# Performance work log

Hardware: AMD Instinct MI355X
Metric: run time of the kernel (lower is better)

## Reference

```python
import jax, jax.numpy as jnp
import numpy as np

N_NODES = 50000
N_EDGES = 800000
IN_DIM = 50
HIDDEN = 256
N_CLASSES = 121
EPS = 1e-12


def setup_inputs() -> dict:
    key = jax.random.key(0)
    ks = jax.random.split(key, 12)
    p = lambda i, shape: (jax.random.normal(ks[i], shape, dtype=jnp.float32) * 0.05)
    x = jax.random.normal(ks[0], (N_NODES, IN_DIM), dtype=jnp.float32)
    edge_index = jax.random.randint(ks[1], (2, N_EDGES), 0, N_NODES, dtype=jnp.int64)
    return {
        "x": x,
        "edge_index": edge_index,
        # SAGEConv layer 1: lin_l (aggregated, with bias), lin_r (root, no bias)
        "w1_l": p(2, (IN_DIM, HIDDEN)), "b1": p(3, (HIDDEN,)), "w1_r": p(4, (IN_DIM, HIDDEN)),
        # parallel Linear 1
        "wl1": p(5, (IN_DIM, HIDDEN)), "bl1": p(6, (HIDDEN,)),
        # SAGEConv layer 2
        "w2_l": p(7, (HIDDEN, N_CLASSES)), "b2": p(8, (N_CLASSES,)), "w2_r": p(9, (HIDDEN, N_CLASSES)),
        # parallel Linear 2
        "wl2": p(10, (HIDDEN, N_CLASSES)), "bl2": p(11, (N_CLASSES,)),
    }


def _sage_conv(x, src, dst, w_l, b, w_r):
    # mean-aggregate source features at destination nodes (PyG SAGEConv, aggr='mean')
    n = x.shape[0]
    agg = jax.ops.segment_sum(x[src], dst, num_segments=n)            # [N, d]
    deg = jax.ops.segment_sum(jnp.ones((src.shape[0], 1), x.dtype), dst, num_segments=n)
    mean = agg / jnp.maximum(deg, 1.0)
    out = mean @ w_l + b + x @ w_r
    # normalize=True -> L2 row normalization (F.normalize semantics)
    norm = jnp.sqrt(jnp.sum(out * out, axis=-1, keepdims=True))
    return out / jnp.maximum(norm, EPS)


def reference(x, edge_index, w1_l, b1, w1_r, wl1, bl1, w2_l, b2, w2_r, wl2, bl2):
    src, dst = edge_index[0], edge_index[1]
    h = jax.nn.elu(_sage_conv(x, src, dst, w1_l, b1, w1_r) + (x @ wl1 + bl1))
    out = _sage_conv(h, src, dst, w2_l, b2, w2_r) + (h @ wl2 + bl2)
    return out
```

## Files before the change

### kernel.cpp

```cpp
#include <hip/hip_runtime.h>
#include <hip/hip_bf16.h>
#include <math.h>

typedef __hip_bfloat16 bf16;
typedef __attribute__((ext_vector_type(8))) short short8;
typedef __attribute__((ext_vector_type(4))) float f32x4;

#define N_NODES 50000
#define N_EDGES 800000
#define IN_DIM 50
#define HIDDEN 256
#define NCLS 121
#define PSTR 128
#define LDSPITCH 264
#define NCHUNK 196
#define P2ROWS 64
#define P1ROWS 32
#define P1PITCH 261
#define FEDGE 1024

#define OFF_OFF   50048
#define OFF_CSR   150160
#define OFF_HB    950272
#define OFF_PB    7350272
#define OFF_AB    10550272
#define OFF_QRB   15000272
#define OFF_QLB   18200272
#define OFF_BW    21400272
#define OFF_BW1   21449424
#define OFF_CSUM  21482240

__device__ __forceinline__ int clampi(int v, int hi) {
    return v < 0 ? 0 : (v >= hi ? hi - 1 : v);
}

__device__ __forceinline__ float uf(unsigned u) { return __uint_as_float(u); }

__global__ __launch_bounds__(256) void prep_r21(
    const float* __restrict__ x, bf16* __restrict__ xbp, bf16* __restrict__ ab,
    const float* __restrict__ w1l, const float* __restrict__ w1r,
    const float* __restrict__ wl1, bf16* __restrict__ bw1,
    const float* __restrict__ w2l, const float* __restrict__ w2r,
    const float* __restrict__ wl2, bf16* __restrict__ bw,
    int* __restrict__ degi) {
    int b = blockIdx.x;
    if (b < 25000) {
        int i = b * 256 + threadIdx.x;
        int n = i >> 7, c = i & 127;
        float v = 0.0f;
        if (c >= 64 && c < 64 + IN_DIM) v = x[n * IN_DIM + (c - 64)];
        ab[i] = __float2bfloat16(v);
        if (c < 64) {
            float xv = (c < IN_DIM) ? x[n * IN_DIM + c] : 0.0f;
            xbp[n * 64 + c] = __float2bfloat16(xv);
        }
    } else if (b < 25256) {
        int i = (b - 25000) * 256 + threadIdx.x;
        int kt = i / 16384, r = i % 16384, c = r / 32, t32 = r % 32;
        int q = t32 >> 3, j = t32 & 7;
        int k = kt * 32 + q * 8 + j;
        float v = 0.0f;
        if (k < 64) {
            if (k < IN_DIM && c < 256) v = w1l[k * HIDDEN + c];
        } else {
            int kr = k - 64;
            if (kr < IN_DIM)
                v = (c < 256) ? w1r[kr * HIDDEN + c] : wl1[kr * HIDDEN + (c - 256)];
        }
        bw1[i] = __float2bfloat16(v);
    } else if (b < 25640) {
        int i = (b - 25256) * 256 + threadIdx.x;
        int kt = i / 12288, r = i % 12288, c = r / 32, t32 = r % 32;
        int q = t32 >> 3, j = t32 & 7;
        int k = kt * 32 + q * 8 + j;
        int mat = c >> 7, cls = c & 127;
        float v = 0.0f;
        if (cls < NCLS) {
            const float* w = (mat == 0) ? w2l : ((mat == 1) ? w2r : wl2);
            v = w[k * NCLS + cls];
        }
        bw[i] = __float2bfloat16(v);
    } else {
        int i = (b - 25640) * 256 + threadIdx.x;
        if (i < N_NODES) degi[i] = 0;
    }
}

__global__ __launch_bounds__(256) void degrank_r21(const int* __restrict__ dst,
                                                   int* __restrict__ degi,
                                                   int* __restrict__ rank) {
    int e = blockIdx.x * 256 + threadIdx.x;
    if (e < N_EDGES) {
        int d = clampi(dst[e], N_NODES);
        rank[e] = atomicAdd(&degi[d], 1);
    }
}

__global__ __launch_bounds__(256) void chunksum_r21(const int* __restrict__ degi,
                                                    int* __restrict__ csum) {
    __shared__ int red[256];
    int i = blockIdx.x * 256 + threadIdx.x;
    red[threadIdx.x] = (i < N_NODES) ? degi[i] : 0;
    __syncthreads();
    for (int s = 128; s > 0; s >>= 1) {
        if (threadIdx.x < s) red[threadIdx.x] += red[threadIdx.x + s];
        __syncthreads();
    }
    if (threadIdx.x == 0) csum[blockIdx.x] = red[0];
}

__global__ __launch_bounds__(256) void scanscatter_r21(const int* __restrict__ csum,
                                                       const int* __restrict__ degi,
                                                       int* __restrict__ off) {
    __shared__ int cs[256];
    __shared__ int s[256];
    int t = threadIdx.x;
    int cv = (t < NCHUNK) ? csum[t] : 0;
    cs[t] = cv;
    __syncthreads();
    for (int d = 1; d < 256; d <<= 1) {
        int u = (t >= d) ? cs[t - d] : 0;
        __syncthreads();
        cs[t] += u;
        __syncthreads();
    }
    int cb = cs[blockIdx.x] - csum[blockIdx.x];
    if (blockIdx.x == 0 && t == 0) off[N_NODES] = cs[NCHUNK - 1];
    int i = blockIdx.x * 256 + t;
    int dv = (i < N_NODES) ? degi[i] : 0;
    s[t] = dv;
    __syncthreads();
    for (int d = 1; d < 256; d <<= 1) {
        int u = (t >= d) ? s[t - d] : 0;
        __syncthreads();
        s[t] += u;
        __syncthreads();
    }
    if (i < N_NODES) off[i] = s[t] - dv + cb;
}

__global__ __launch_bounds__(256) void csrfill2_r21(const int* __restrict__ src,
                                                    const int* __restrict__ dst,
                                                    const int* __restrict__ rank,
                                                    const int* __restrict__ off,
                                                    int* __restrict__ csr) {
    int e = blockIdx.x * 256 + threadIdx.x;
    if (e >= N_EDGES) return;
    int d = clampi(dst[e], N_NODES);
    csr[off[d] + rank[e]] = clampi(src[e], N_NODES);
}

__global__ __launch_bounds__(256) void gather1_r21(
    const uint2* __restrict__ xb2, const int* __restrict__ off,
    const int* __restrict__ csr, const int* __restrict__ degi,
    unsigned int* __restrict__ abu) {
    __shared__ float rdeg[8];
    __shared__ int soff[9];
    __shared__ int sidx[FEDGE];
    int base = blockIdx.x * 8;
    int tid = threadIdx.x;
    if (tid < 9) soff[tid] = off[base + tid];
    if (tid < 8) rdeg[tid] = 1.0f / fmaxf((float)degi[base + tid], 1.0f);
    __syncthreads();
    int e0b = soff[0];
    int count = soff[8] - e0b;
    bool inl = (count <= FEDGE);
    if (inl)
        for (int i = tid; i < count; i += 256) sidx[i] = csr[e0b + i];
    __syncthreads();

    int wave = tid >> 6, lane = tid & 63;
    int half = lane >> 5;
    int grp = (lane >> 4) & 1;
    int lg = lane & 15;
    int n = wave * 2 + half;
    int node = base + n;
    int e0 = soff[n], e1 = soff[n + 1];
    float a0 = 0, a1 = 0, a2 = 0, a3 = 0;
    float b0 = 0, b1 = 0, b2 = 0, b3 = 0;
    int e = e0;
    for (; e + 4 <= e1; e += 4) {
        int r0 = inl ? sidx[e + grp - e0b] : csr[e + grp];
        int r1 = inl ? sidx[e + 2 + grp - e0b] : csr[e + 2 + grp];
        uint2 u0 = xb2[(size_t)r0 * 16 + lg];
        uint2 u1 = xb2[(size_t)r1 * 16 + lg];
        a0 += uf(u0.x << 16);
        a1 += uf(u0.x & 0xffff0000u);
        a2 += uf(u0.y << 16);
        a3 += uf(u0.y & 0xffff0000u);
        b0 += uf(u1.x << 16);
        b1 += uf(u1.x & 0xffff0000u);
        b2 += uf(u1.y << 16);
        b3 += uf(u1.y & 0xffff0000u);
    }
    for (; e < e1; e += 2) {
        int idx = e + grp;
        int safe = idx < e1 ? idx : e;
        int r0 = inl ? sidx[safe - e0b] : csr[safe];
        uint2 u0 = xb2[(size_t)r0 * 16 + lg];
        if (idx < e1) {
            a0 += uf(u0.x << 16);
            a1 += uf(u0.x & 0xffff0000u);
            a2 += uf(u0.y << 16);
            a3 += uf(u0.y & 0xffff0000u);
        }
    }
    a0 += b0;
    a1 += b1;
    a2 += b2;
    a3 += b3;
    a0 += __shfl_xor(a0, 16, 64);
    a1 += __shfl_xor(a1, 16, 64);
    a2 += __shfl_xor(a2, 16, 64);
    a3 += __shfl_xor(a3, 16, 64);
    if (grp == 0) {
        float r = rdeg[n];
        bf16 v0 = __float2bfloat16(a0 * r), v1 = __float2bfloat16(a1 * r);
        bf16 v2 = __float2bfloat16(a2 * r), v3 = __float2bfloat16(a3 * r);
        unsigned p0 = (unsigned)*(unsigned short*)&v0 |
                      ((unsigned)*(unsigned short*)&v1 << 16);
        unsigned p1 = (unsigned)*(unsigned short*)&v2 |
                      ((unsigned)*(unsigned short*)&v3 << 16);
        abu[(size_t)node * 64 + 2 * lg] = p0;
        abu[(size_t)node * 64 + 2 * lg + 1] = p1;
    }
}

__global__ __launch_bounds__(256) void proj1_r21(
    const bf16* __restrict__ ab_, const bf16* __restrict__ bw1,
    const float* __restrict__ b1, const float* __restrict__ bl1,
    bf16* __restrict__ hb) {
    __shared__ float osA[P1ROWS][P1PITCH];
    __shared__ short osB[P1ROWS][256];
    __shared__ float partial[P1ROWS][9];
    __shared__ float rns[P1ROWS];

    int base = blockIdx.x * P1ROWS;
    int tid = threadIdx.x;
    int wave = tid >> 6, lane = tid & 63;
    int rc = lane & 15, quad = lane >> 4;

    const short* ab = (const short*)ab_;
    short8 af[2][4];
#pragma unroll
    for (int rg = 0; rg < 2; ++rg)
#pragma unroll
        for (int kt = 0; kt < 4; ++kt)
            af[rg][kt] = *(const short8*)
                &ab[(size_t)(base + rg * 16 + rc) * 128 + kt * 32 + quad * 8];

    const short* bws = (const short*)bw1;
    for (int ti = 0; ti < 8; ++ti) {
        int t = wave * 8 + ti;
        f32x4 acc[2] = {{0, 0, 0, 0}, {0, 0, 0, 0}};
#pragma unroll
        for (int kt = 0; kt < 4; ++kt) {
            short8 bf = *(const short8*)
                &bws[(((size_t)kt * 512 + t * 16 + rc) * 4 + quad) * 8];
#pragma unroll
            for (int rg = 0; rg < 2; ++rg)
                acc[rg] = __builtin_amdgcn_mfma_f32_16x16x32_bf16(af[rg][kt], bf,
                                                                  acc[rg], 0, 0, 0);
        }
        int col = t * 16 + rc;
        if (col < 256) {
#pragma unroll
            for (int rg = 0; rg < 2; ++rg)
#pragma unroll
                for (int r = 0; r < 4; ++r)
                    osA[rg * 16 + quad * 4 + r][col] = acc[rg][r];
        } else {
#pragma unroll
            for (int rg = 0; rg < 2; ++rg)
#pragma unroll
                for (int r = 0; r < 4; ++r) {
                    bf16 v = __float2bfloat16(acc[rg][r]);
                    osB[rg * 16 + quad * 4 + r][col - 256] = *(short*)&v;
                }
        }
    }
    __syncthreads();
    {
        int n = tid & 31, jj = tid >> 5;
        float s = 0.0f;
#pragma unroll
        for (int c = 0; c < 32; ++c) {
            int cc = jj * 32 + c;
            float v = osA[n][cc] + b1[cc];
            s += v * v;
        }
        partial[n][jj] = s;
    }
    __syncthreads();
    if (tid < 32) {
        float s = 0.0f;
#pragma unroll
        for (int jj = 0; jj < 8; ++jj) s += partial[tid][jj];
        rns[tid] = 1.0f / fmaxf(sqrtf(s), 1e-12f);
    }
    __syncthreads();
    for (int i = 0; i < 32; ++i) {
        int idx = i * 256 + tid;
        int n = idx >> 8, c = idx & 255;
        int node = base + n;
        if (node < N_NODES) {
            short sb = osB[n][c];
            float lin = __bfloat162float(*(bf16*)&sb);
            float z = (osA[n][c] + b1[c]) * rns[n] + lin + bl1[c];
            hb[(size_t)node * HIDDEN + c] =
                __float2bfloat16(z > 0.0f ? z : expm1f(z));
        }
    }
}

__global__ __launch_bounds__(256) void proj2_r21(
    const bf16* __restrict__ hb, const bf16* __restrict__ bw,
    bf16* __restrict__ pb, bf16* __restrict__ qrb, bf16* __restrict__ qlb) {
    __shared__ __align__(16) short hs[P2ROWS * LDSPITCH];

    int base = blockIdx.x * P2ROWS;
    int tid = threadIdx.x;
    const short* hbs = (const short*)hb;
#pragma unroll
    for (int i = 0; i < 8; ++i) {
        int f = tid + 256 * i;
        int row = f >> 5, u4 = f & 31;
        *(uint4*)&hs[row * LDSPITCH + u4 * 8] =
            *(const uint4*)(hbs + (size_t)(base + row) * HIDDEN + u4 * 8);
    }
    __syncthreads();

    int wave = tid >> 6, lane = tid & 63;
    int rc = lane & 15, quad = lane >> 4;

    short8 af[4][8];
#pragma unroll
    for (int rg = 0; rg < 4; ++rg)
#pragma unroll
        for (int kt = 0; kt < 8; ++kt)
            af[rg][kt] = *(const short8*)
                &hs[(rg * 16 + rc) * LDSPITCH + kt * 32 + quad * 8];

    const short* bws = (const short*)bw;
    for (int ti = 0; ti < 6; ++ti) {
        int t = wave * 6 + ti;
        f32x4 acc[4] = {{0, 0, 0, 0}, {0, 0, 0, 0}, {0, 0, 0, 0}, {0, 0, 0, 0}};
#pragma unroll
        for (int kt = 0; kt < 8; ++kt) {
            short8 bf = *(const short8*)
                &bws[(((size_t)kt * 384 + t * 16 + rc) * 4 + quad) * 8];
#pragma unroll
            for (int rg = 0; rg < 4; ++rg)
                acc[rg] = __builtin_amdgcn_mfma_f32_16x16x32_bf16(af[rg][kt], bf,
                                                                  acc[rg], 0, 0, 0);
        }
        int col = t * 16 + rc;
        int mat = col >> 7, cls = col & 127;
        bf16* dstp = (mat == 0) ? pb : ((mat == 1) ? qrb : qlb);
#pragma unroll
        for (int rg = 0; rg < 4; ++rg)
#pragma unroll
            for (int r = 0; r < 4; ++r) {
                int node = base + rg * 16 + quad * 4 + r;
                if (node < N_NODES)
                    dstp[(size_t)node * PSTR + cls] = __float2bfloat16(acc[rg][r]);
            }
    }
}

__global__ __launch_bounds__(256) void final_r21(
    const bf16* __restrict__ pb, const bf16* __restrict__ qrb,
    const bf16* __restrict__ qlb, const int* __restrict__ off,
    const int* __restrict__ csr, const int* __restrict__ degi,
    const float* __restrict__ b2, const float* __restrict__ bl2,
    float* __restrict__ out) {
    __shared__ float mp[8][128];
    __shared__ float red[8][128];
    __shared__ float rdeg[8];
    __shared__ int soff[9];
    __shared__ int sidx[FEDGE];

    const uint4* pbu4 = (const uint4*)pb;
    int base = blockIdx.x * 8;
    int tid = threadIdx.x;
    if (tid < 9) soff[tid] = off[base + tid];
    if (tid < 8) rdeg[tid] = 1.0f / fmaxf((float)degi[base + tid], 1.0f);
    __syncthreads();
    int e0b = soff[0];
    int count = soff[8] - e0b;
    bool inl = (count <= FEDGE);
    if (inl)
        for (int i = tid; i < count; i += 256) sidx[i] = csr[e0b + i];
    __syncthreads();

    int wv = tid >> 6, lane = tid & 63;
    int g = lane >> 4, lg = lane & 15;
#pragma unroll
    for (int i = 0; i < 2; ++i) {
        int n = wv * 2 + i;
        int e0 = soff[n], e1 = soff[n + 1];
        float a[8] = {0, 0, 0, 0, 0, 0, 0, 0};
        float b[8] = {0, 0, 0, 0, 0, 0, 0, 0};
        int e = e0;
        for (; e + 8 <= e1; e += 8) {
            int r0 = inl ? sidx[e + g - e0b] : csr[e + g];
            int r1 = inl ? sidx[e + 4 + g - e0b] : csr[e + 4 + g];
            uint4 u0 = pbu4[(size_t)r0 * 16 + lg];
            uint4 u1 = pbu4[(size_t)r1 * 16 + lg];
            a[0] += uf(u0.x << 16);
            a[1] += uf(u0.x & 0xffff0000u);
            a[2] += uf(u0.y << 16);
            a[3] += uf(u0.y & 0xffff0000u);
            a[4] += uf(u0.z << 16);
            a[5] += uf(u0.z & 0xffff0000u);
            a[6] += uf(u0.w << 16);
            a[7] += uf(u0.w & 0xffff0000u);
            b[0] += uf(u1.x << 16);
            b[1] += uf(u1.x & 0xffff0000u);
            b[2] += uf(u1.y << 16);
            b[3] += uf(u1.y & 0xffff0000u);
            b[4] += uf(u1.z << 16);
            b[5] += uf(u1.z & 0xffff0000u);
            b[6] += uf(u1.w << 16);
            b[7] += uf(u1.w & 0xffff0000u);
        }
        for (; e < e1; e += 4) {
            int idx = e + g;
            int safe = idx < e1 ? idx : e;
            int r0 = inl ? sidx[safe - e0b] : csr[safe];
            uint4 u0 = pbu4[(size_t)r0 * 16 + lg];
            if (idx < e1) {
                a[0] += uf(u0.x << 16);
                a[1] += uf(u0.x & 0xffff0000u);
                a[2] += uf(u0.y << 16);
                a[3] += uf(u0.y & 0xffff0000u);
                a[4] += uf(u0.z << 16);
                a[5] += uf(u0.z & 0xffff0000u);
                a[6] += uf(u0.w << 16);
                a[7] += uf(u0.w & 0xffff0000u);
            }
        }
#pragma unroll
        for (int k = 0; k < 8; ++k) a[k] += b[k];
#pragma unroll
        for (int k = 0; k < 8; ++k) {
            a[k] += __shfl_xor(a[k], 16, 64);
            a[k] += __shfl_xor(a[k], 32, 64);
        }
        if (g == 0) {
#pragma unroll
            for (int k = 0; k < 8; ++k) mp[n][8 * lg + k] = a[k];
        }
    }
    __syncthreads();

    int j = tid & 127, gg = tid >> 7;
    float bj = (j < NCLS) ? b2[j] : 0.0f;
    float blj = (j < NCLS) ? bl2[j] : 0.0f;
    float out2[4];
#pragma unroll
    for (int i = 0; i < 4; ++i) {
        int n = gg * 4 + i;
        out2[i] = (j < NCLS)
                      ? (mp[n][j] * rdeg[n] + bj +
                         __bfloat162float(qrb[(size_t)(base + n) * PSTR + j]))
                      : 0.0f;
        red[n][j] = out2[i] * out2[i];
    }
    __syncthreads();
    for (int stride = 64; stride > 0; stride >>= 1) {
        if (j < stride) {
#pragma unroll
            for (int i = 0; i < 4; ++i)
                red[gg * 4 + i][j] += red[gg * 4 + i][j + stride];
        }
        __syncthreads();
    }
    if (j < NCLS) {
#pragma unroll
        for (int i = 0; i < 4; ++i) {
            int n = gg * 4 + i;
            float rn = 1.0f / fmaxf(sqrtf(red[n][0]), 1e-12f);
            out[(base + n) * NCLS + j] =
                out2[i] * rn +
                __bfloat162float(qlb[(size_t)(base + n) * PSTR + j]) + blj;
        }
    }
}

extern "C" void kernel_launch(void* const* d_in, const int* in_sizes, int n_in,
                              void* d_out, int out_size, void* d_ws, size_t ws_size,
                              hipStream_t stream) {
    const float* x   = (const float*)d_in[0];
    const int*   ei  = (const int*)d_in[1];
    const float* w1l = (const float*)d_in[2];
    const float* b1  = (const float*)d_in[3];
    const float* w1r = (const float*)d_in[4];
    const float* wl1 = (const float*)d_in[5];
    const float* bl1 = (const float*)d_in[6];
    const float* w2l = (const float*)d_in[7];
    const float* b2  = (const float*)d_in[8];
    const float* w2r = (const float*)d_in[9];
    const float* wl2 = (const float*)d_in[10];
    const float* bl2 = (const float*)d_in[11];
    float* out = (float*)d_out;

    const int* src = ei;
    const int* dst = ei + N_EDGES;

    int*   wsI   = (int*)d_ws;
    float* wsF   = (float*)d_ws;
    int*   degi  = wsI;
    int*   off   = wsI + OFF_OFF;
    int*   csr   = wsI + OFF_CSR;
    bf16*  hb    = (bf16*)(wsF + OFF_HB);
    int*   rank  = (int*)(wsF + OFF_HB);
    bf16*  pb    = (bf16*)(wsF + OFF_PB);
    bf16*  xbp   = (bf16*)(wsF + OFF_PB);
    bf16*  ab    = (bf16*)(wsF + OFF_AB);
    bf16*  qrb   = (bf16*)(wsF + OFF_QRB);
    bf16*  qlb   = (bf16*)(wsF + OFF_QLB);
    bf16*  bw    = (bf16*)(wsF + OFF_BW);
    bf16*  bw1   = (bf16*)(wsF + OFF_BW1);
    int*   csum  = wsI + OFF_CSUM;

    prep_r21<<<25836, 256, 0, stream>>>(x, xbp, ab, w1l, w1r, wl1, bw1,
                                        w2l, w2r, wl2, bw, degi);

    degrank_r21<<<(N_EDGES + 255) / 256, 256, 0, stream>>>(dst, degi, rank);

    chunksum_r21<<<NCHUNK, 256, 0, stream>>>(degi, csum);
    scanscatter_r21<<<NCHUNK, 256, 0, stream>>>(csum, degi, off);

    csrfill2_r21<<<(N_EDGES + 255) / 256, 256, 0, stream>>>(src, dst, rank, off, csr);

    gather1_r21<<<N_NODES / 8, 256, 0, stream>>>((const uint2*)xbp, off,
                                                 csr, degi, (unsigned int*)ab);
    proj1_r21<<<(N_NODES + P1ROWS - 1) / P1ROWS, 256, 0, stream>>>(ab, bw1, b1, bl1, hb);
    proj2_r21<<<(N_NODES + P2ROWS - 1) / P2ROWS, 256, 0, stream>>>(hb, bw, pb, qrb, qlb);
    final_r21<<<N_NODES / 8, 256, 0, stream>>>(pb, qrb, qlb,
                                               off, csr, degi, b2, bl2, out);
}
```

Baseline: 290.6 us.

## Rewrite proj1 as register-resident per-wave epilogue without LDS staging

The first-layer projection kernel now gives each wave 16 rows and computes all 256 SAGE output columns in registers. The L2 row norm is reduced with cross-lane shuffles, and the parallel-linear columns are computed and fused straight into the ELU epilogue. This drops the LDS staging buffers, three block barriers and the bf16 round-trip of the linear branch. In exchange it raises register pressure (16 accumulators per thread) and writes hb with scattered 2-byte stores.

```diff
diff --git a/kernel.cpp b/kernel.cpp
--- a/kernel.cpp
+++ b/kernel.cpp
@@ -15,8 +15,6 @@
 #define LDSPITCH 264
 #define NCHUNK 196
 #define P2ROWS 64
-#define P1ROWS 32
-#define P1PITCH 261
 #define FEDGE 1024
 
 #define OFF_OFF   50048
@@ -36,7 +34,7 @@
 
 __device__ __forceinline__ float uf(unsigned u) { return __uint_as_float(u); }
 
-__global__ __launch_bounds__(256) void prep_r21(
+__global__ __launch_bounds__(256) void prep_r22(
     const float* __restrict__ x, bf16* __restrict__ xbp, bf16* __restrict__ ab,
     const float* __restrict__ w1l, const float* __restrict__ w1r,
     const float* __restrict__ wl1, bf16* __restrict__ bw1,
@@ -86,7 +84,7 @@
     }
 }
 
-__global__ __launch_bounds__(256) void degrank_r21(const int* __restrict__ dst,
+__global__ __launch_bounds__(256) void degrank_r22(const int* __restrict__ dst,
                                                    int* __restrict__ degi,
                                                    int* __restrict__ rank) {
     int e = blockIdx.x * 256 + threadIdx.x;
@@ -96,7 +94,7 @@
     }
 }
 
-__global__ __launch_bounds__(256) void chunksum_r21(const int* __restrict__ degi,
+__global__ __launch_bounds__(256) void chunksum_r22(const int* __restrict__ degi,
                                                     int* __restrict__ csum) {
     __shared__ int red[256];
     int i = blockIdx.x * 256 + threadIdx.x;
@@ -109,7 +107,7 @@
     if (threadIdx.x == 0) csum[blockIdx.x] = red[0];
 }
 
-__global__ __launch_bounds__(256) void scanscatter_r21(const int* __restrict__ csum,
+__global__ __launch_bounds__(256) void scanscatter_r22(const int* __restrict__ csum,
                                                        const int* __restrict__ degi,
                                                        int* __restrict__ off) {
     __shared__ int cs[256];
@@ -139,7 +137,7 @@
     if (i < N_NODES) off[i] = s[t] - dv + cb;
 }
 
-__global__ __launch_bounds__(256) void csrfill2_r21(const int* __restrict__ src,
+__global__ __launch_bounds__(256) void csrfill2_r22(const int* __restrict__ src,
                                                     const int* __restrict__ dst,
                                                     const int* __restrict__ rank,
                                                     const int* __restrict__ off,
@@ -150,7 +148,7 @@
     csr[off[d] + rank[e]] = clampi(src[e], N_NODES);
 }
 
-__global__ __launch_bounds__(256) void gather1_r21(
+__global__ __launch_bounds__(256) void gather1_r22(
     const uint2* __restrict__ xb2, const int* __restrict__ off,
     const int* __restrict__ csr, const int* __restrict__ degi,
     unsigned int* __restrict__ abu) {
@@ -226,94 +224,95 @@
     }
 }
 
-__global__ __launch_bounds__(256) void proj1_r21(
+__global__ __launch_bounds__(256) void proj1_r22(
     const bf16* __restrict__ ab_, const bf16* __restrict__ bw1,
     const float* __restrict__ b1, const float* __restrict__ bl1,
     bf16* __restrict__ hb) {
-    __shared__ float osA[P1ROWS][P1PITCH];
-    __shared__ short osB[P1ROWS][256];
-    __shared__ float partial[P1ROWS][9];
-    __shared__ float rns[P1ROWS];
-
-    int base = blockIdx.x * P1ROWS;
     int tid = threadIdx.x;
     int wave = tid >> 6, lane = tid & 63;
     int rc = lane & 15, quad = lane >> 4;
+    int rowbase = blockIdx.x * 64 + wave * 16;
 
     const short* ab = (const short*)ab_;
-    short8 af[2][4];
-#pragma unroll
-    for (int rg = 0; rg < 2; ++rg)
-#pragma unroll
-        for (int kt = 0; kt < 4; ++kt)
-            af[rg][kt] = *(const short8*)
-                &ab[(size_t)(base + rg * 16 + rc) * 128 + kt * 32 + quad * 8];
+    short8 af[4];
+#pragma unroll
+    for (int kt = 0; kt < 4; ++kt)
+        af[kt] = *(const short8*)
+            &ab[(size_t)(rowbase + rc) * 128 + kt * 32 + quad * 8];
 
     const short* bws = (const short*)bw1;
-    for (int ti = 0; ti < 8; ++ti) {
-        int t = wave * 8 + ti;
-        f32x4 acc[2] = {{0, 0, 0, 0}, {0, 0, 0, 0}};
+    f32x4 accA[16];
+#pragma unroll
+    for (int ti = 0; ti < 16; ++ti) {
+        f32x4 acc = {0.0f, 0.0f, 0.0f, 0.0f};
 #pragma unroll
         for (int kt = 0; kt < 4; ++kt) {
             short8 bf = *(const short8*)
-                &bws[(((size_t)kt * 512 + t * 16 + rc) * 4 + quad) * 8];
-#pragma unroll
-            for (int rg = 0; rg < 2; ++rg)
-                acc[rg] = __builtin_amdgcn_mfma_f32_16x16x32_bf16(af[rg][kt], bf,
-                                                                  acc[rg], 0, 0, 0);
-        }
-        int col = t * 16 + rc;
-        if (col < 256) {
-#pragma unroll
-            for (int rg = 0; rg < 2; ++rg)
-#pragma unroll
-                for (int r = 0; r < 4; ++r)
-                    osA[rg * 16 + quad * 4 + r][col] = acc[rg][r];
+                &bws[(((size_t)kt * 512 + ti * 16 + rc) * 4 + quad) * 8];
+            acc = __builtin_amdgcn_mfma_f32_16x16x32_bf16(af[kt], bf, acc, 0, 0, 0);
+        }
+        accA[ti] = acc;
+    }
+    float s0 = 0, s1 = 0, s2 = 0, s3 = 0;
+#pragma unroll
+    for (int ti = 0; ti < 16; ++ti) {
+        float bb = b1[ti * 16 + rc];
+        accA[ti][0] += bb;
+        accA[ti][1] += bb;
+        accA[ti][2] += bb;
+        accA[ti][3] += bb;
+        s0 += accA[ti][0] * accA[ti][0];
+        s1 += accA[ti][1] * accA[ti][1];
+        s2 += accA[ti][2] * accA[ti][2];
+        s3 += accA[ti][3] * accA[ti][3];
+    }
+#pragma unroll
+    for (int m = 1; m < 16; m <<= 1) {
+        s0 += __shfl_xor(s0, m, 64);
+        s1 += __shfl_xor(s1, m, 64);
+        s2 += __shfl_xor(s2, m, 64);
+        s3 += __shfl_xor(s3, m, 64);
+    }
+    float rn0 = 1.0f / fmaxf(sqrtf(s0), 1e-12f);
+    float rn1 = 1.0f / fmaxf(sqrtf(s1), 1e-12f);
+    float rn2 = 1.0f / fmaxf(sqrtf(s2), 1e-12f);
+    float rn3 = 1.0f / fmaxf(sqrtf(s3), 1e-12f);
+
+#pragma unroll
+    for (int ti = 0; ti < 16; ++ti) {
+        f32x4 accB = {0.0f, 0.0f, 0.0f, 0.0f};
+#pragma unroll
+        for (int kt = 0; kt < 4; ++kt) {
+            short8 bf = *(const short8*)
+                &bws[(((size_t)kt * 512 + (16 + ti) * 16 + rc) * 4 + quad) * 8];
+            accB = __builtin_amdgcn_mfma_f32_16x16x32_bf16(af[kt], bf, accB, 0, 0, 0);
+        }
+        int c = ti * 16 + rc;
+        float blv = bl1[c];
+        float z0 = accA[ti][0] * rn0 + accB[0] + blv;
+        float z1 = accA[ti][1] * rn1 + accB[1] + blv;
+        float z2 = accA[ti][2] * rn2 + accB[2] + blv;
+        float z3 = accA[ti][3] * rn3 + accB[3] + blv;
+        z0 = z0 > 0.0f ? z0 : expm1f(z0);
+        z1 = z1 > 0.0f ? z1 : expm1f(z1);
+        z2 = z2 > 0.0f ? z2 : expm1f(z2);
+        z3 = z3 > 0.0f ? z3 : expm1f(z3);
+        int row = rowbase + quad * 4;
+        if (row + 3 < N_NODES) {
+            hb[(size_t)(row + 0) * HIDDEN + c] = __float2bfloat16(z0);
+            hb[(size_t)(row + 1) * HIDDEN + c] = __float2bfloat16(z1);
+            hb[(size_t)(row + 2) * HIDDEN + c] = __float2bfloat16(z2);
+            hb[(size_t)(row + 3) * HIDDEN + c] = __float2bfloat16(z3);
         } else {
-#pragma unroll
-            for (int rg = 0; rg < 2; ++rg)
-#pragma unroll
-                for (int r = 0; r < 4; ++r) {
-                    bf16 v = __float2bfloat16(acc[rg][r]);
-                    osB[rg * 16 + quad * 4 + r][col - 256] = *(short*)&v;
-                }
-        }
-    }
-    __syncthreads();
-    {
-        int n = tid & 31, jj = tid >> 5;
-        float s = 0.0f;
-#pragma unroll
-        for (int c = 0; c < 32; ++c) {
-            int cc = jj * 32 + c;
-            float v = osA[n][cc] + b1[cc];
-            s += v * v;
-        }
-        partial[n][jj] = s;
-    }
-    __syncthreads();
-    if (tid < 32) {
-        float s = 0.0f;
-#pragma unroll
-        for (int jj = 0; jj < 8; ++jj) s += partial[tid][jj];
-        rns[tid] = 1.0f / fmaxf(sqrtf(s), 1e-12f);
-    }
-    __syncthreads();
-    for (int i = 0; i < 32; ++i) {
-        int idx = i * 256 + tid;
-        int n = idx >> 8, c = idx & 255;
-        int node = base + n;
-        if (node < N_NODES) {
-            short sb = osB[n][c];
-            float lin = __bfloat162float(*(bf16*)&sb);
-            float z = (osA[n][c] + b1[c]) * rns[n] + lin + bl1[c];
-            hb[(size_t)node * HIDDEN + c] =
-                __float2bfloat16(z > 0.0f ? z : expm1f(z));
-        }
-    }
-}
-
-__global__ __launch_bounds__(256) void proj2_r21(
+            if (row + 0 < N_NODES) hb[(size_t)(row + 0) * HIDDEN + c] = __float2bfloat16(z0);
+            if (row + 1 < N_NODES) hb[(size_t)(row + 1) * HIDDEN + c] = __float2bfloat16(z1);
+            if (row + 2 < N_NODES) hb[(size_t)(row + 2) * HIDDEN + c] = __float2bfloat16(z2);
+            if (row + 3 < N_NODES) hb[(size_t)(row + 3) * HIDDEN + c] = __float2bfloat16(z3);
+        }
+    }
+}
+
+__global__ __launch_bounds__(256) void proj2_r22(
     const bf16* __restrict__ hb, const bf16* __restrict__ bw,
     bf16* __restrict__ pb, bf16* __restrict__ qrb, bf16* __restrict__ qlb) {
     __shared__ __align__(16) short hs[P2ROWS * LDSPITCH];
@@ -368,7 +367,7 @@
     }
 }
 
-__global__ __launch_bounds__(256) void final_r21(
+__global__ __launch_bounds__(256) void final_r22(
     const bf16* __restrict__ pb, const bf16* __restrict__ qrb,
     const bf16* __restrict__ qlb, const int* __restrict__ off,
     const int* __restrict__ csr, const int* __restrict__ degi,
@@ -524,20 +523,20 @@
     bf16*  bw1   = (bf16*)(wsF + OFF_BW1);
     int*   csum  = wsI + OFF_CSUM;
 
-    prep_r21<<<25836, 256, 0, stream>>>(x, xbp, ab, w1l, w1r, wl1, bw1,
+    prep_r22<<<25836, 256, 0, stream>>>(x, xbp, ab, w1l, w1r, wl1, bw1,
                                         w2l, w2r, wl2, bw, degi);
 
-    degrank_r21<<<(N_EDGES + 255) / 256, 256, 0, stream>>>(dst, degi, rank);
-
-    chunksum_r21<<<NCHUNK, 256, 0, stream>>>(degi, csum);
-    scanscatter_r21<<<NCHUNK, 256, 0, stream>>>(csum, degi, off);
-
-    csrfill2_r21<<<(N_EDGES + 255) / 256, 256, 0, stream>>>(src, dst, rank, off, csr);
-
-    gather1_r21<<<N_NODES / 8, 256, 0, stream>>>((const uint2*)xbp, off,
+    degrank_r22<<<(N_EDGES + 255) / 256, 256, 0, stream>>>(dst, degi, rank);
+
+    chunksum_r22<<<NCHUNK, 256, 0, stream>>>(degi, csum);
+    scanscatter_r22<<<NCHUNK, 256, 0, stream>>>(csum, degi, off);
+
+    csrfill2_r22<<<(N_EDGES + 255) / 256, 256, 0, stream>>>(src, dst, rank, off, csr);
+
+    gather1_r22<<<N_NODES / 8, 256, 0, stream>>>((const uint2*)xbp, off,
                                                  csr, degi, (unsigned int*)ab);
-    proj1_r21<<<(N_NODES + P1ROWS - 1) / P1ROWS, 256, 0, stream>>>(ab, bw1, b1, bl1, hb);
-    proj2_r21<<<(N_NODES + P2ROWS - 1) / P2ROWS, 256, 0, stream>>>(hb, bw, pb, qrb, qlb);
-    final_r21<<<N_NODES / 8, 256, 0, stream>>>(pb, qrb, qlb,
+    proj1_r22<<<(N_NODES + 63) / 64, 256, 0, stream>>>(ab, bw1, b1, bl1, hb);
+    proj2_r22<<<(N_NODES + P2ROWS - 1) / P2ROWS, 256, 0, stream>>>(hb, bw, pb, qrb, qlb);
+    final_r22<<<N_NODES / 8, 256, 0, stream>>>(pb, qrb, qlb,
                                                off, csr, degi, b2, bl2, out);
 }
```

New measurement: 290.9 us. Within noise of the previous version (+0.1%).

## Restructure layer-1 projection to keep outputs in registers and normalize via shuffles

Applied to the files above, without the earlier changes.

The layer-1 projection kernel now handles 64 rows per block, stages the A tile in LDS, and keeps the SAGE-branch accumulators in registers. The row L2 norm is reduced with cross-lane shuffles plus a small per-wave partial table, replacing the large fp32/bf16 LDS output staging and the separate reduction passes. The linear branch is then computed per column group and fused directly into the ELU epilogue. This cuts LDS traffic and barriers, at the cost of higher register pressure from 16 accumulator vectors per lane and uncoalesced 2-byte column-strided stores to hb.

```diff
diff --git a/kernel.cpp b/kernel.cpp
--- a/kernel.cpp
+++ b/kernel.cpp
@@ -15,8 +15,7 @@
 #define LDSPITCH 264
 #define NCHUNK 196
 #define P2ROWS 64
-#define P1ROWS 32
-#define P1PITCH 261
+#define P1PITCH 136
 #define FEDGE 1024
 
 #define OFF_OFF   50048
@@ -36,7 +35,7 @@
 
 __device__ __forceinline__ float uf(unsigned u) { return __uint_as_float(u); }
 
-__global__ __launch_bounds__(256) void prep_r21(
+__global__ __launch_bounds__(256) void prep_r23(
     const float* __restrict__ x, bf16* __restrict__ xbp, bf16* __restrict__ ab,
     const float* __restrict__ w1l, const float* __restrict__ w1r,
     const float* __restrict__ wl1, bf16* __restrict__ bw1,
@@ -86,7 +85,7 @@
     }
 }
 
-__global__ __launch_bounds__(256) void degrank_r21(const int* __restrict__ dst,
+__global__ __launch_bounds__(256) void degrank_r23(const int* __restrict__ dst,
                                                    int* __restrict__ degi,
                                                    int* __restrict__ rank) {
     int e = blockIdx.x * 256 + threadIdx.x;
@@ -96,7 +95,7 @@
     }
 }
 
-__global__ __launch_bounds__(256) void chunksum_r21(const int* __restrict__ degi,
+__global__ __launch_bounds__(256) void chunksum_r23(const int* __restrict__ degi,
                                                     int* __restrict__ csum) {
     __shared__ int red[256];
     int i = blockIdx.x * 256 + threadIdx.x;
@@ -109,7 +108,7 @@
     if (threadIdx.x == 0) csum[blockIdx.x] = red[0];
 }
 
-__global__ __launch_bounds__(256) void scanscatter_r21(const int* __restrict__ csum,
+__global__ __launch_bounds__(256) void scanscatter_r23(const int* __restrict__ csum,
                                                        const int* __restrict__ degi,
                                                        int* __restrict__ off) {
     __shared__ int cs[256];
@@ -139,7 +138,7 @@
     if (i < N_NODES) off[i] = s[t] - dv + cb;
 }
 
-__global__ __launch_bounds__(256) void csrfill2_r21(const int* __restrict__ src,
+__global__ __launch_bounds__(256) void csrfill2_r23(const int* __restrict__ src,
                                                     const int* __restrict__ dst,
                                                     const int* __restrict__ rank,
                                                     const int* __restrict__ off,
@@ -150,7 +149,7 @@
     csr[off[d] + rank[e]] = clampi(src[e], N_NODES);
 }
 
-__global__ __launch_bounds__(256) void gather1_r21(
+__global__ __launch_bounds__(256) void gather1_r23(
     const uint2* __restrict__ xb2, const int* __restrict__ off,
     const int* __restrict__ csr, const int* __restrict__ degi,
     unsigned int* __restrict__ abu) {
@@ -226,94 +225,126 @@
     }
 }
 
-__global__ __launch_bounds__(256) void proj1_r21(
+__global__ __launch_bounds__(256) void proj1_r23(
     const bf16* __restrict__ ab_, const bf16* __restrict__ bw1,
     const float* __restrict__ b1, const float* __restrict__ bl1,
     bf16* __restrict__ hb) {
-    __shared__ float osA[P1ROWS][P1PITCH];
-    __shared__ short osB[P1ROWS][256];
-    __shared__ float partial[P1ROWS][9];
-    __shared__ float rns[P1ROWS];
-
-    int base = blockIdx.x * P1ROWS;
+    __shared__ __align__(16) short as_[64 * P1PITCH];
+    __shared__ float part[4][64];
+
+    int base = blockIdx.x * 64;
     int tid = threadIdx.x;
+    const short* abs_ = (const short*)ab_;
+#pragma unroll
+    for (int i = 0; i < 4; ++i) {
+        int c = tid + 256 * i;
+        int row = c >> 4, u = c & 15;
+        *(uint4*)&as_[row * P1PITCH + u * 8] =
+            *(const uint4*)(abs_ + (size_t)(base + row) * 128 + u * 8);
+    }
+    __syncthreads();
+
     int wave = tid >> 6, lane = tid & 63;
     int rc = lane & 15, quad = lane >> 4;
-
-    const short* ab = (const short*)ab_;
-    short8 af[2][4];
-#pragma unroll
-    for (int rg = 0; rg < 2; ++rg)
-#pragma unroll
-        for (int kt = 0; kt < 4; ++kt)
-            af[rg][kt] = *(const short8*)
-                &ab[(size_t)(base + rg * 16 + rc) * 128 + kt * 32 + quad * 8];
-
     const short* bws = (const short*)bw1;
-    for (int ti = 0; ti < 8; ++ti) {
-        int t = wave * 8 + ti;
-        f32x4 acc[2] = {{0, 0, 0, 0}, {0, 0, 0, 0}};
-#pragma unroll
-        for (int kt = 0; kt < 4; ++kt) {
+
+    f32x4 acc[4][4];
+#pragma unroll
+    for (int p = 0; p < 4; ++p)
+#pragma unroll
+        for (int rg = 0; rg < 4; ++rg) acc[p][rg] = (f32x4){0, 0, 0, 0};
+#pragma unroll
+    for (int kt = 0; kt < 4; ++kt) {
+        short8 a0 = *(const short8*)&as_[(0 * 16 + rc) * P1PITCH + kt * 32 + quad * 8];
+        short8 a1 = *(const short8*)&as_[(1 * 16 + rc) * P1PITCH + kt * 32 + quad * 8];
+        short8 a2 = *(const short8*)&as_[(2 * 16 + rc) * P1PITCH + kt * 32 + quad * 8];
+        short8 a3 = *(const short8*)&as_[(3 * 16 + rc) * P1PITCH + kt * 32 + quad * 8];
+#pragma unroll
+        for (int p = 0; p < 4; ++p) {
+            int t = wave * 4 + p;
             short8 bf = *(const short8*)
                 &bws[(((size_t)kt * 512 + t * 16 + rc) * 4 + quad) * 8];
-#pragma unroll
-            for (int rg = 0; rg < 2; ++rg)
-                acc[rg] = __builtin_amdgcn_mfma_f32_16x16x32_bf16(af[rg][kt], bf,
-                                                                  acc[rg], 0, 0, 0);
-        }
-        int col = t * 16 + rc;
-        if (col < 256) {
-#pragma unroll
-            for (int rg = 0; rg < 2; ++rg)
-#pragma unroll
-                for (int r = 0; r < 4; ++r)
-                    osA[rg * 16 + quad * 4 + r][col] = acc[rg][r];
-        } else {
-#pragma unroll
-            for (int rg = 0; rg < 2; ++rg)
-#pragma unroll
-                for (int r = 0; r < 4; ++r) {
-                    bf16 v = __float2bfloat16(acc[rg][r]);
-                    osB[rg * 16 + quad * 4 + r][col - 256] = *(short*)&v;
-                }
-        }
-    }
-    __syncthreads();
-    {
-        int n = tid & 31, jj = tid >> 5;
-        float s = 0.0f;
-#pragma unroll
-        for (int c = 0; c < 32; ++c) {
-            int cc = jj * 32 + c;
-            float v = osA[n][cc] + b1[cc];
-            s += v * v;
-        }
-        partial[n][jj] = s;
-    }
-    __syncthreads();
-    if (tid < 32) {
-        float s = 0.0f;
-#pragma unroll
-        for (int jj = 0; jj < 8; ++jj) s += partial[tid][jj];
-        rns[tid] = 1.0f / fmaxf(sqrtf(s), 1e-12f);
-    }
-    __syncthreads();
-    for (int i = 0; i < 32; ++i) {
-        int idx = i * 256 + tid;
-        int n = idx >> 8, c = idx & 255;
-        int node = base + n;
-        if (node < N_NODES) {
-            short sb = osB[n][c];
-            float lin = __bfloat162float(*(bf16*)&sb);
-            float z = (osA[n][c] + b1[c]) * rns[n] + lin + bl1[c];
-            hb[(size_t)node * HIDDEN + c] =
-                __float2bfloat16(z > 0.0f ? z : expm1f(z));
-        }
-    }
-}
-
-__global__ __launch_bounds__(256) void proj2_r21(
+            acc[p][0] = __builtin_amdgcn_mfma_f32_16x16x32_bf16(a0, bf, acc[p][0], 0, 0, 0);
+            acc[p][1] = __builtin_amdgcn_mfma_f32_16x16x32_bf16(a1, bf, acc[p][1], 0, 0, 0);
+            acc[p][2] = __builtin_amdgcn_mfma_f32_16x16x32_bf16(a2, bf, acc[p][2], 0, 0, 0);
+            acc[p][3] = __builtin_amdgcn_mfma_f32_16x16x32_bf16(a3, bf, acc[p][3], 0, 0, 0);
+        }
+    }
+    float sq[4][4];
+#pragma unroll
+    for (int rg = 0; rg < 4; ++rg)
+#pragma unroll
+        for (int r = 0; r < 4; ++r) sq[rg][r] = 0.0f;
+#pragma unroll
+    for (int p = 0; p < 4; ++p) {
+        float bb = b1[(wave * 4 + p) * 16 + rc];
+#pragma unroll
+        for (int rg = 0; rg < 4; ++rg)
+#pragma unroll
+            for (int r = 0; r < 4; ++r) {
+                acc[p][rg][r] += bb;
+                sq[rg][r] += acc[p][rg][r] * acc[p][rg][r];
+            }
+    }
+#pragma unroll
+    for (int m = 1; m < 16; m <<= 1)
+#pragma unroll
+        for (int rg = 0; rg < 4; ++rg)
+#pragma unroll
+            for (int r = 0; r < 4; ++r) sq[rg][r] += __shfl_xor(sq[rg][r], m, 64);
+    if (rc == 0) {
+#pragma unroll
+        for (int rg = 0; rg < 4; ++rg)
+#pragma unroll
+            for (int r = 0; r < 4; ++r)
+                part[wave][rg * 16 + quad * 4 + r] = sq[rg][r];
+    }
+    __syncthreads();
+    float rns[4][4];
+#pragma unroll
+    for (int rg = 0; rg < 4; ++rg)
+#pragma unroll
+        for (int r = 0; r < 4; ++r) {
+            int row = rg * 16 + quad * 4 + r;
+            float s = part[0][row] + part[1][row] + part[2][row] + part[3][row];
+            rns[rg][r] = 1.0f / fmaxf(sqrtf(s), 1e-12f);
+        }
+
+#pragma unroll
+    for (int p = 0; p < 4; ++p) {
+        int t = 16 + wave * 4 + p;
+        f32x4 accB[4];
+#pragma unroll
+        for (int rg = 0; rg < 4; ++rg) accB[rg] = (f32x4){0, 0, 0, 0};
+#pragma unroll
+        for (int kt = 0; kt < 4; ++kt) {
+            short8 a0 = *(const short8*)&as_[(0 * 16 + rc) * P1PITCH + kt * 32 + quad * 8];
+            short8 a1 = *(const short8*)&as_[(1 * 16 + rc) * P1PITCH + kt * 32 + quad * 8];
+            short8 a2 = *(const short8*)&as_[(2 * 16 + rc) * P1PITCH + kt * 32 + quad * 8];
+            short8 a3 = *(const short8*)&as_[(3 * 16 + rc) * P1PITCH + kt * 32 + quad * 8];
+            short8 bf = *(const short8*)
+                &bws[(((size_t)kt * 512 + t * 16 + rc) * 4 + quad) * 8];
+            accB[0] = __builtin_amdgcn_mfma_f32_16x16x32_bf16(a0, bf, accB[0], 0, 0, 0);
+            accB[1] = __builtin_amdgcn_mfma_f32_16x16x32_bf16(a1, bf, accB[1], 0, 0, 0);
+            accB[2] = __builtin_amdgcn_mfma_f32_16x16x32_bf16(a2, bf, accB[2], 0, 0, 0);
+            accB[3] = __builtin_amdgcn_mfma_f32_16x16x32_bf16(a3, bf, accB[3], 0, 0, 0);
+        }
+        int c = (wave * 4 + p) * 16 + rc;
+        float blv = bl1[c];
+#pragma unroll
+        for (int rg = 0; rg < 4; ++rg)
+#pragma unroll
+            for (int r = 0; r < 4; ++r) {
+                float z = acc[p][rg][r] * rns[rg][r] + accB[rg][r] + blv;
+                z = z > 0.0f ? z : expm1f(z);
+                int row = base + rg * 16 + quad * 4 + r;
+                if (row < N_NODES)
+                    hb[(size_t)row * HIDDEN + c] = __float2bfloat16(z);
+            }
+    }
+}
+
+__global__ __launch_bounds__(256) void proj2_r23(
     const bf16* __restrict__ hb, const bf16* __restrict__ bw,
     bf16* __restrict__ pb, bf16* __restrict__ qrb, bf16* __restrict__ qlb) {
     __shared__ __align__(16) short hs[P2ROWS * LDSPITCH];
@@ -368,7 +399,7 @@
     }
 }
 
-__global__ __launch_bounds__(256) void final_r21(
+__global__ __launch_bounds__(256) void final_r23(
     const bf16* __restrict__ pb, const bf16* __restrict__ qrb,
     const bf16* __restrict__ qlb, const int* __restrict__ off,
     const int* __restrict__ csr, const int* __restrict__ degi,
@@ -524,20 +555,20 @@
     bf16*  bw1   = (bf16*)(wsF + OFF_BW1);
     int*   csum  = wsI + OFF_CSUM;
 
-    prep_r21<<<25836, 256, 0, stream>>>(x, xbp, ab, w1l, w1r, wl1, bw1,
+    prep_r23<<<25836, 256, 0, stream>>>(x, xbp, ab, w1l, w1r, wl1, bw1,
                                         w2l, w2r, wl2, bw, degi);
 
-    degrank_r21<<<(N_EDGES + 255) / 256, 256, 0, stream>>>(dst, degi, rank);
-
-    chunksum_r21<<<NCHUNK, 256, 0, stream>>>(degi, csum);
-    scanscatter_r21<<<NCHUNK, 256, 0, stream>>>(csum, degi, off);
-
-    csrfill2_r21<<<(N_EDGES + 255) / 256, 256, 0, stream>>>(src, dst, rank, off, csr);
-
-    gather1_r21<<<N_NODES / 8, 256, 0, stream>>>((const uint2*)xbp, off,
+    degrank_r23<<<(N_EDGES + 255) / 256, 256, 0, stream>>>(dst, degi, rank);
+
+    chunksum_r23<<<NCHUNK, 256, 0, stream>>>(degi, csum);
+    scanscatter_r23<<<NCHUNK, 256, 0, stream>>>(csum, degi, off);
+
+    csrfill2_r23<<<(N_EDGES + 255) / 256, 256, 0, stream>>>(src, dst, rank, off, csr);
+
+    gather1_r23<<<N_NODES / 8, 256, 0, stream>>>((const uint2*)xbp, off,
                                                  csr, degi, (unsigned int*)ab);
-    proj1_r21<<<(N_NODES + P1ROWS - 1) / P1ROWS, 256, 0, stream>>>(ab, bw1, b1, bl1, hb);
-    proj2_r21<<<(N_NODES + P2ROWS - 1) / P2ROWS, 256, 0, stream>>>(hb, bw, pb, qrb, qlb);
-    final_r21<<<N_NODES / 8, 256, 0, stream>>>(pb, qrb, qlb,
+    proj1_r23<<<(N_NODES + 63) / 64, 256, 0, stream>>>(ab, bw1, b1, bl1, hb);
+    proj2_r23<<<(N_NODES + P2ROWS - 1) / P2ROWS, 256, 0, stream>>>(hb, bw, pb, qrb, qlb);
+    final_r23<<<N_NODES / 8, 256, 0, stream>>>(pb, qrb, qlb,
                                                off, csr, degi, b2, bl2, out);
 }
```

New measurement: 296.1 us. No clear change (+1.9%).
